# Kernel tuning notes

Measured on AMD Instinct MI355X. Metric: run time of the kernel, lower is better.

## Reference

```python
import jax, jax.numpy as jnp
import numpy as np

N, E, B = 250000, 1000000, 500
FD = 78  # num_features_xd


def setup_inputs() -> dict:
    key = jax.random.key(0)
    ks = jax.random.split(key, 24)
    g = lambda i, shape, fan_in: jax.random.normal(ks[i], shape, jnp.float32) / np.sqrt(fan_in)
    inp = {
        "x": jax.random.normal(ks[0], (N, FD), jnp.float32),
        "edge_index": jax.random.randint(ks[1], (2, E), 0, N, jnp.int32),
        "batch": jnp.repeat(jnp.arange(B, dtype=jnp.int32), N // B),  # sorted, every graph non-empty
        "target": jax.random.randint(ks[2], (B, 1000), 0, 26, jnp.int32),
        # GCN layers
        "W1": g(3, (FD, FD), FD), "b1": jnp.zeros((FD,), jnp.float32),
        "W2": g(4, (FD, 2 * FD), FD), "b2": jnp.zeros((2 * FD,), jnp.float32),
        "W3": g(5, (2 * FD, 4 * FD), 2 * FD), "b3": jnp.zeros((4 * FD,), jnp.float32),
        # graph head
        "fcg1_w": g(6, (4 * FD, 1024), 4 * FD), "fcg1_b": jnp.zeros((1024,), jnp.float32),
        "fcg2_w": g(7, (1024, 128), 1024), "fcg2_b": jnp.zeros((128,), jnp.float32),
        # protein branch
        "emb": g(8, (26, 128), 1),
        "conv_w": g(9, (32, 1000, 8), 1000 * 8), "conv_b": jnp.zeros((32,), jnp.float32),
        "fcxt_w": g(10, (32 * 121, 128), 32 * 121), "fcxt_b": jnp.zeros((128,), jnp.float32),
        # fusion head
        "fc1_w": g(11, (256, 1024), 256), "fc1_b": jnp.zeros((1024,), jnp.float32),
        "fc2_w": g(12, (1024, 512), 1024), "fc2_b": jnp.zeros((512,), jnp.float32),
        "out_w": g(13, (512, 1), 512), "out_b": jnp.zeros((1,), jnp.float32),
    }
    return inp


def _gcn_conv(x, W, b, src, dst, dinv, n):
    # PyG GCNConv: out = D^-1/2 (A+I) D^-1/2 (x W) + b, symmetric norm with self-loops
    xw = x @ W
    norm = dinv[src] * dinv[dst]                                   # [E]
    agg = jax.ops.segment_sum(xw[src] * norm[:, None], dst, num_segments=n)
    agg = agg + xw * (dinv * dinv)[:, None]                        # self-loop term
    return agg + b


def reference(x, edge_index, batch, target,
              W1, b1, W2, b2, W3, b3,
              fcg1_w, fcg1_b, fcg2_w, fcg2_b,
              emb, conv_w, conv_b, fcxt_w, fcxt_b,
              fc1_w, fc1_b, fc2_w, fc2_b, out_w, out_b):
    n = x.shape[0]
    src, dst = edge_index[0], edge_index[1]
    # degree with self-loops (edge weights 1)
    deg = jax.ops.segment_sum(jnp.ones((src.shape[0],), x.dtype), dst, num_segments=n) + 1.0
    dinv = jax.lax.rsqrt(deg)

    h = jax.nn.relu(_gcn_conv(x, W1, b1, src, dst, dinv, n))
    h = jax.nn.relu(_gcn_conv(h, W2, b2, src, dst, dinv, n))
    h = jax.nn.relu(_gcn_conv(h, W3, b3, src, dst, dinv, n))

    bsz = fcg2_w.shape[1] * 0 + target.shape[0]  # B
    g = jax.ops.segment_max(h, batch, num_segments=bsz)            # global max pool -> [B, 312]
    g = jax.nn.relu(g @ fcg1_w + fcg1_b)
    g = g @ fcg2_w + fcg2_b                                        # dropout = identity (eval)

    # protein branch: Conv1d over embedding dim (channels = seq positions = 1000)
    e = emb[target]                                                # [B, 1000, 128]
    c = jax.lax.conv_general_dilated(e, conv_w, window_strides=(1,), padding="VALID",
                                     dimension_numbers=("NCH", "OIH", "NCH"))
    c = c + conv_b[None, :, None]                                  # [B, 32, 121]
    xt = c.reshape(bsz, 32 * 121) @ fcxt_w + fcxt_b

    xc = jnp.concatenate([g, xt], axis=1)                          # [B, 256]
    xc = jax.nn.relu(xc @ fc1_w + fc1_b)
    xc = jax.nn.relu(xc @ fc2_w + fc2_b)
    return xc @ out_w + out_b                                      # [B, 1]
```

## Files before the change

### kernel.cpp

```cpp
#include <hip/hip_runtime.h>
#include <hip/hip_bf16.h>

#define DEV_INLINE __device__ __forceinline__

static constexpr int Nn = 250000;
static constexpr int Ee = 1000000;
static constexpr int Bb = 500;
static constexpr int NPB = Nn / Bb;

typedef __attribute__((ext_vector_type(8))) short short8;
typedef __attribute__((ext_vector_type(8))) unsigned short ushort8v;
typedef __attribute__((ext_vector_type(4))) float f32x4;

DEV_INLINE float b2f(__hip_bfloat16 v) { return __bfloat162float(v); }
DEV_INLINE __hip_bfloat16 f2b(float v) { return __float2bfloat16(v); }
DEV_INLINE unsigned short f2bu(float v) {
    __hip_bfloat16 h = __float2bfloat16(v);
    return __builtin_bit_cast(unsigned short, h);
}
DEV_INLINE float bfu2f(unsigned short u) { return __uint_as_float(((unsigned)u) << 16); }

__global__ void k_deg(const int* __restrict__ dst, int* __restrict__ deg) {
    int i = blockIdx.x * 256 + threadIdx.x;
    if (i < Ee) atomicAdd(&deg[dst[i]], 1);
}

__global__ void k_dinv(const int* __restrict__ deg, float* __restrict__ dinv) {
    int i = blockIdx.x * 256 + threadIdx.x;
    if (i < Nn) dinv[i] = rsqrtf((float)deg[i] + 1.0f);
}

__global__ __launch_bounds__(256) void k_scan1(const int* __restrict__ deg,
                                               int* __restrict__ rp,
                                               int* __restrict__ bsum) {
    __shared__ int s[256];
    int t = threadIdx.x;
    int i = blockIdx.x * 256 + t;
    int v = (i < Nn) ? deg[i] : 0;
    s[t] = v;
    __syncthreads();
    for (int off = 1; off < 256; off <<= 1) {
        int x = (t >= off) ? s[t - off] : 0;
        __syncthreads();
        s[t] += x;
        __syncthreads();
    }
    if (i < Nn) rp[i] = s[t] - v;
    if (t == 255) bsum[blockIdx.x] = s[255];
}

__global__ __launch_bounds__(1024) void k_scan2(int* __restrict__ bsum, int nb) {
    __shared__ int s[1024];
    int t = threadIdx.x;
    int v = (t < nb) ? bsum[t] : 0;
    s[t] = v;
    __syncthreads();
    for (int off = 1; off < 1024; off <<= 1) {
        int x = (t >= off) ? s[t - off] : 0;
        __syncthreads();
        s[t] += x;
        __syncthreads();
    }
    if (t < nb) bsum[t] = s[t] - v;
}

__global__ void k_scan3(int* __restrict__ rp, int* __restrict__ cursor,
                        const int* __restrict__ bsum) {
    int i = blockIdx.x * 256 + threadIdx.x;
    if (i < Nn) {
        int v = rp[i] + bsum[blockIdx.x];
        rp[i] = v;
        cursor[i] = v;
    }
    if (i == 0) rp[Nn] = Ee;
}

__global__ void k_scatter(const int* __restrict__ src, const int* __restrict__ dst,
                          const float* __restrict__ dinv, int* __restrict__ cursor,
                          int* __restrict__ col, float* __restrict__ enorm) {
    int i = blockIdx.x * 256 + threadIdx.x;
    if (i >= Ee) return;
    int s = src[i], d = dst[i];
    int pos = atomicAdd(&cursor[d], 1);
    col[pos] = s;
    enorm[pos] = dinv[s] * dinv[d];
}

__global__ void k_xprep(const float* __restrict__ x, unsigned short* __restrict__ xb) {
    int gid = blockIdx.x * 256 + threadIdx.x;
    if (gid >= Nn * 20) return;
    int i = gid / 20;
    int c = gid - 20 * i;
    int k = 4 * c;
    const float* xp = x + (size_t)i * 78;
    ushort4 u;
    u.x = (k + 0 < 78) ? f2bu(xp[k + 0]) : (unsigned short)0;
    u.y = (k + 1 < 78) ? f2bu(xp[k + 1]) : (unsigned short)0;
    u.z = (k + 2 < 78) ? f2bu(xp[k + 2]) : (unsigned short)0;
    u.w = (k + 3 < 78) ? f2bu(xp[k + 3]) : (unsigned short)0;
    *(ushort4*)&xb[(size_t)i * 80 + k] = u;
}

template <int K, int F, int KP, int FP>
__global__ __launch_bounds__(64) void k_wprep(const float* __restrict__ W,
                                              unsigned short* __restrict__ Wb) {
    constexpr int KSTEPS = KP / 32;
    const int nt = blockIdx.x, ks = blockIdx.y;
    const int l = threadIdx.x;
    const int n = nt * 16 + (l & 15);
    unsigned short* o = Wb + ((size_t)(nt * KSTEPS + ks) * 64 + l) * 8;
#pragma unroll
    for (int j = 0; j < 8; ++j) {
        const int k = (l >> 4) * 8 + j + ks * 32;
        o[j] = (k < K && n < F) ? f2bu(W[(size_t)k * F + n]) : (unsigned short)0;
    }
}

template <int KIN, int KP, int F, int FP, int SOUT, bool POOL>
__global__ __launch_bounds__(320) void k_gcn(const __hip_bfloat16* __restrict__ in_,
                                             const int* __restrict__ rp,
                                             const int* __restrict__ col,
                                             const float* __restrict__ enorm,
                                             const float* __restrict__ dinv,
                                             const unsigned short* __restrict__ Wb,
                                             const float* __restrict__ bias,
                                             __hip_bfloat16* __restrict__ out,
                                             float* __restrict__ gpool) {
    constexpr int ROWS = 16, BD = 320, WAVES = 5;
    constexpr int CPR = KIN / 8;
    constexpr int SLOTS = CPR * ROWS;
    constexpr int ECAP = 16 * ROWS;
    constexpr int KSTEPS = KP / 32;
    constexpr int NT = FP / 16;
    constexpr int TPW = NT / WAVES;
    static_assert(KIN % 8 == 0 && KP % 32 == 0 && KP >= KIN && FP % (16 * WAVES) == 0, "pad");
    const unsigned short* in = (const unsigned short*)in_;

    __shared__ alignas(16) unsigned short sh[ROWS * KP];
    __shared__ int sRp[ROWS + 1];
    __shared__ int sCol[ECAP];
    __shared__ float sEn[ECAP];

    const int i0 = blockIdx.x * ROWS;
    const int t = threadIdx.x;

    if (t <= ROWS) sRp[t] = rp[i0 + t];
    const int base = rp[i0];
    const int ne = rp[i0 + ROWS] - base;
    if (ne <= ECAP) {
        for (int e = t; e < ne; e += BD) {
            sCol[e] = col[base + e];
            sEn[e] = enorm[base + e];
        }
    }
    if constexpr (KP > KIN) {
        for (int e = t; e < ROWS * (KP - KIN); e += BD) {
            const int r = e / (KP - KIN);
            sh[r * KP + KIN + (e - r * (KP - KIN))] = 0;
        }
    }
    __syncthreads();

    for (int slot = t; slot < SLOTS; slot += BD) {
        const int r = slot / CPR;
        const int c = slot - r * CPR;
        const int i = i0 + r;
        const size_t coff = (size_t)8 * c;
        const float di = dinv[i];
        const float selfw = di * di;
        float acc[8];
        {
            ushort8v s = *(const ushort8v*)(in + (size_t)i * KIN + coff);
#pragma unroll
            for (int j = 0; j < 8; ++j) acc[j] = bfu2f(s[j]) * selfw;
        }
        const int e0a = sRp[r], e1a = sRp[r + 1];
        if (ne <= ECAP) {
            int j = e0a - base;
            const int jend = e1a - base;
            for (; j + 4 <= jend; j += 4) {
                const int n0 = sCol[j + 0], n1 = sCol[j + 1], n2 = sCol[j + 2], n3 = sCol[j + 3];
                const float w0 = sEn[j + 0], w1 = sEn[j + 1], w2 = sEn[j + 2], w3 = sEn[j + 3];
                ushort8v a0 = *(const ushort8v*)(in + (size_t)n0 * KIN + coff);
                ushort8v a1 = *(const ushort8v*)(in + (size_t)n1 * KIN + coff);
                ushort8v a2 = *(const ushort8v*)(in + (size_t)n2 * KIN + coff);
                ushort8v a3 = *(const ushort8v*)(in + (size_t)n3 * KIN + coff);
#pragma unroll
                for (int q = 0; q < 8; ++q)
                    acc[q] += bfu2f(a0[q]) * w0 + bfu2f(a1[q]) * w1 +
                              bfu2f(a2[q]) * w2 + bfu2f(a3[q]) * w3;
            }
            for (; j < jend; ++j) {
                const int n = sCol[j];
                const float w = sEn[j];
                ushort8v a = *(const ushort8v*)(in + (size_t)n * KIN + coff);
#pragma unroll
                for (int q = 0; q < 8; ++q) acc[q] += bfu2f(a[q]) * w;
            }
        } else {
            for (int j = e0a; j < e1a; ++j) {
                const int n = col[j];
                const float w = enorm[j];
                ushort8v a = *(const ushort8v*)(in + (size_t)n * KIN + coff);
#pragma unroll
                for (int q = 0; q < 8; ++q) acc[q] += bfu2f(a[q]) * w;
            }
        }
        ushort8v o;
#pragma unroll
        for (int q = 0; q < 8; ++q) o[q] = f2bu(acc[q]);
        *(ushort8v*)&sh[r * KP + 8 * c] = o;
    }
    __syncthreads();

    const int w = t >> 6, lane = t & 63;
    const int arow = lane & 15, aquad = lane >> 4;
    short8 afr[KSTEPS];
#pragma unroll
    for (int ks = 0; ks < KSTEPS; ++ks)
        afr[ks] = *(const short8*)&sh[arow * KP + aquad * 8 + ks * 32];

    const bool uni = (i0 / NPB) == ((i0 + ROWS - 1) / NPB);

#pragma unroll
    for (int nti = 0; nti < TPW; ++nti) {
        const int nt = w * TPW + nti;
        const short8* bp = (const short8*)Wb + (size_t)nt * KSTEPS * 64 + lane;
        f32x4 acc = {0.f, 0.f, 0.f, 0.f};
#pragma unroll
        for (int ks = 0; ks < KSTEPS; ++ks) {
            short8 bfr = bp[ks * 64];
            acc = __builtin_amdgcn_mfma_f32_16x16x32_bf16(afr[ks], bfr, acc, 0, 0, 0);
        }
        const int f = nt * 16 + arow;
        const int ib = i0 + aquad * 4;
        if constexpr (!POOL) {
            if (f < F) {
                const float bv = bias[f];
#pragma unroll
                for (int r = 0; r < 4; ++r)
                    out[(size_t)(ib + r) * SOUT + f] = f2b(fmaxf(acc[r] + bv, 0.f));
            } else if (f < SOUT) {
#pragma unroll
                for (int r = 0; r < 4; ++r)
                    out[(size_t)(ib + r) * SOUT + f] = f2b(0.f);
            }
        } else {
            float m = 0.f, v[4];
            const float bv = (f < F) ? bias[f] : 0.f;
#pragma unroll
            for (int r = 0; r < 4; ++r) {
                v[r] = fmaxf(acc[r] + bv, 0.f);
                m = fmaxf(m, v[r]);
            }
            if (uni) {
                m = fmaxf(m, __shfl_xor(m, 16));
                m = fmaxf(m, __shfl_xor(m, 32));
                if (aquad == 0 && f < F)
                    atomicMax((int*)&gpool[(i0 / NPB) * F + f], __float_as_int(m));
            } else if (f < F) {
                const int g0 = ib / NPB, g3 = (ib + 3) / NPB;
                if (g0 == g3) {
                    atomicMax((int*)&gpool[g0 * F + f], __float_as_int(m));
                } else {
#pragma unroll
                    for (int r = 0; r < 4; ++r)
                        atomicMax((int*)&gpool[((ib + r) / NPB) * F + f], __float_as_int(v[r]));
                }
            }
        }
    }
}

template <int K, int FOUT, int KS, bool RELU, int BD>
__global__ __launch_bounds__(BD) void k_fc(const float* __restrict__ in,
                                           const float* __restrict__ W,
                                           const float* __restrict__ bias,
                                           float* __restrict__ out,
                                           int ostride, int ooff) {
    static_assert(!(RELU && KS > 1), "cannot split K with fused ReLU");
    static_assert(K % KS == 0, "K must divide evenly");
    constexpr int KC = K / KS;
    const int j = blockIdx.x * BD + threadIdx.x;
    const int b = blockIdx.y;
    const int z = blockIdx.z;
    const float* __restrict__ inp = in + (size_t)b * K + z * KC;
    const float* __restrict__ Wp = W + (size_t)(z * KC) * FOUT + j;
    float acc = (z == 0) ? bias[j] : 0.f;
#pragma unroll 8
    for (int k = 0; k < KC; ++k) acc += inp[k] * Wp[(size_t)k * FOUT];
    float* dst = &out[(size_t)b * ostride + ooff + j];
    if (KS > 1) {
        atomicAdd(dst, acc);
    } else {
        *dst = RELU ? fmaxf(acc, 0.f) : acc;
    }
}

__global__ __launch_bounds__(128) void k_P(const float* __restrict__ emb,
                                           const float* __restrict__ fcxt_w,
                                           float* __restrict__ P) {
    const int v = blockIdx.x, o = blockIdx.y;
    const int j = threadIdx.x;
    __shared__ float se[128];
    se[j] = emb[v * 128 + j];
    __syncthreads();
    float acc[8];
#pragma unroll
    for (int k = 0; k < 8; ++k) acc[k] = 0.f;
    const float* fw = fcxt_w + (size_t)(o * 121) * 128 + j;
#pragma unroll 4
    for (int h = 0; h < 121; ++h) {
        const float f = fw[(size_t)h * 128];
#pragma unroll
        for (int k = 0; k < 8; ++k) acc[k] += se[h + k] * f;
    }
    float* Pp = P + ((size_t)(v * 32 + o) * 8) * 128 + j;
#pragma unroll
    for (int k = 0; k < 8; ++k) Pp[(size_t)k * 128] = acc[k];
}

__global__ __launch_bounds__(128) void k_T(const float* __restrict__ convw,
                                           const float* __restrict__ P,
                                           float* __restrict__ T) {
    const int i0 = blockIdx.x * 8;
    const int v = blockIdx.y;
    const int t = threadIdx.x;
    __shared__ float wt[8 * 256];
    for (int e = t; e < 2048; e += 128) {
        const int r = e >> 8;
        const int kk = e & 255;
        wt[e] = convw[(size_t)(kk >> 3) * 8000 + (size_t)(i0 + r) * 8 + (kk & 7)];
    }
    __syncthreads();
    float acc[8];
#pragma unroll
    for (int r = 0; r < 8; ++r) acc[r] = 0.f;
    const float* Pp = P + (size_t)v * 256 * 128 + t;
#pragma unroll 2
    for (int kk = 0; kk < 256; ++kk) {
        const float pv = Pp[(size_t)kk * 128];
#pragma unroll
        for (int r = 0; r < 8; ++r) acc[r] += wt[r * 256 + kk] * pv;
    }
    float* Tp = T + ((size_t)v * 1000 + i0) * 128 + t;
#pragma unroll
    for (int r = 0; r < 8; ++r) Tp[(size_t)r * 128] = acc[r];
}

__global__ __launch_bounds__(128) void k_C0(const float* __restrict__ fcxt_w,
                                            const float* __restrict__ fcxt_b,
                                            const float* __restrict__ convb,
                                            float* __restrict__ C0) {
    const int o = blockIdx.x;
    const int j = threadIdx.x;
    float acc = 0.f;
    const float* fw = fcxt_w + (size_t)(o * 121) * 128 + j;
#pragma unroll 4
    for (int h = 0; h < 121; ++h) acc += fw[(size_t)h * 128];
    acc *= convb[o];
    if (o == 0) acc += fcxt_b[j];
    atomicAdd(&C0[j], acc);
}

template <int ZS>
__global__ __launch_bounds__(128) void k_xt(const int* __restrict__ target,
                                            const float* __restrict__ T,
                                            const float* __restrict__ C0,
                                            float* __restrict__ xc) {
    constexpr int CH = 1000 / ZS;
    const int b = blockIdx.x;
    const int z = blockIdx.y;
    const int j = threadIdx.x;
    const int* tg = target + b * 1000 + z * CH;
    float acc = (z == 0) ? C0[j] : 0.f;
    int i = 0;
    for (; i + 4 <= CH; i += 4) {
        const int v0 = tg[i + 0], v1 = tg[i + 1], v2 = tg[i + 2], v3 = tg[i + 3];
        const int ib = z * CH + i;
        acc += T[((size_t)v0 * 1000 + ib + 0) * 128 + j]
             + T[((size_t)v1 * 1000 + ib + 1) * 128 + j]
             + T[((size_t)v2 * 1000 + ib + 2) * 128 + j]
             + T[((size_t)v3 * 1000 + ib + 3) * 128 + j];
    }
    for (; i < CH; ++i) {
        acc += T[((size_t)tg[i] * 1000 + z * CH + i) * 128 + j];
    }
    atomicAdd(&xc[(size_t)b * 256 + 128 + j], acc);
}

__global__ __launch_bounds__(64) void k_out(const float* __restrict__ in,
                                            const float* __restrict__ w,
                                            const float* __restrict__ ob,
                                            float* __restrict__ out) {
    const int b = blockIdx.x;
    const int lane = threadIdx.x;
    const float* p = in + (size_t)b * 512;
    float acc = 0.f;
#pragma unroll
    for (int i = 0; i < 8; ++i) acc += p[lane + 64 * i] * w[lane + 64 * i];
    for (int off = 32; off > 0; off >>= 1) acc += __shfl_down(acc, off);
    if (lane == 0) out[b] = acc + ob[0];
}

extern "C" void kernel_launch(void* const* d_in, const int* in_sizes, int n_in,
                              void* d_out, int out_size, void* d_ws, size_t ws_size,
                              hipStream_t stream) {
    (void)in_sizes; (void)n_in; (void)out_size; (void)ws_size;
    const float* x      = (const float*)d_in[0];
    const int* ei       = (const int*)d_in[1];
    const int* target   = (const int*)d_in[3];
    const float* W1     = (const float*)d_in[4];
    const float* b1     = (const float*)d_in[5];
    const float* W2     = (const float*)d_in[6];
    const float* b2     = (const float*)d_in[7];
    const float* W3     = (const float*)d_in[8];
    const float* b3     = (const float*)d_in[9];
    const float* fcg1_w = (const float*)d_in[10];
    const float* fcg1_b = (const float*)d_in[11];
    const float* fcg2_w = (const float*)d_in[12];
    const float* fcg2_b = (const float*)d_in[13];
    const float* emb    = (const float*)d_in[14];
    const float* conv_w = (const float*)d_in[15];
    const float* conv_b = (const float*)d_in[16];
    const float* fcxt_w = (const float*)d_in[17];
    const float* fcxt_b = (const float*)d_in[18];
    const float* fc1_w  = (const float*)d_in[19];
    const float* fc1_b  = (const float*)d_in[20];
    const float* fc2_w  = (const float*)d_in[21];
    const float* fc2_b  = (const float*)d_in[22];
    const float* out_w  = (const float*)d_in[23];
    const float* out_b  = (const float*)d_in[24];

    const int* src = ei;
    const int* dst = ei + Ee;

    size_t off = 0;
    auto alloc = [&](size_t bytes) -> void* {
        off = (off + 255) & ~(size_t)255;
        void* p = (char*)d_ws + off;
        off += bytes;
        return p;
    };
    int*   deg    = (int*)alloc((size_t)Nn * 4);
    float* dinv   = (float*)alloc((size_t)Nn * 4);
    int*   rp     = (int*)alloc((size_t)(Nn + 1) * 4);
    int*   col    = (int*)alloc((size_t)Ee * 4);
    float* enorm  = (float*)alloc((size_t)Ee * 4);
    int*   bsum   = (int*)alloc(1024 * 4);
    unsigned short* Wb1 = (unsigned short*)alloc((size_t)5 * 3 * 64 * 8 * 2);
    unsigned short* Wb2 = (unsigned short*)alloc((size_t)10 * 3 * 64 * 8 * 2);
    unsigned short* Wb3 = (unsigned short*)alloc((size_t)20 * 5 * 64 * 8 * 2);
    __hip_bfloat16* h1 = (__hip_bfloat16*)alloc((size_t)Nn * 80 * 2);
    __hip_bfloat16* h2 = (__hip_bfloat16*)alloc((size_t)Nn * 160 * 2);
    int* cursor = deg;
    unsigned short* xb = (unsigned short*)h2;

    size_t hoff = 0;
    auto halloc = [&](size_t bytes) -> void* {
        hoff = (hoff + 255) & ~(size_t)255;
        void* p = (char*)h1 + hoff;
        hoff += bytes;
        return p;
    };
    float* gpool = (float*)halloc((size_t)Bb * 312 * 4);
    float* g1    = (float*)halloc((size_t)Bb * 1024 * 4);
    float* xc    = (float*)halloc((size_t)Bb * 256 * 4);
    float* f1    = (float*)halloc((size_t)Bb * 1024 * 4);
    float* f2    = (float*)halloc((size_t)Bb * 512 * 4);
    float* C0    = (float*)halloc(128 * 4);
    float* Pbuf  = (float*)halloc((size_t)26 * 32 * 8 * 128 * 4);
    float* Tbuf  = (float*)halloc((size_t)26 * 1000 * 128 * 4);

    const int nb = (Nn + 255) / 256;

    k_xprep<<<(Nn * 20 + 255) / 256, 256, 0, stream>>>(x, xb);

    hipMemsetAsync(deg, 0, (size_t)Nn * 4, stream);
    k_deg<<<(Ee + 255) / 256, 256, 0, stream>>>(dst, deg);
    k_dinv<<<nb, 256, 0, stream>>>(deg, dinv);
    k_scan1<<<nb, 256, 0, stream>>>(deg, rp, bsum);
    k_scan2<<<1, 1024, 0, stream>>>(bsum, nb);
    k_scan3<<<nb, 256, 0, stream>>>(rp, cursor, bsum);
    k_scatter<<<(Ee + 255) / 256, 256, 0, stream>>>(src, dst, dinv, cursor, col, enorm);

    k_wprep<78, 78, 96, 80><<<dim3(5, 3), 64, 0, stream>>>(W1, Wb1);
    k_wprep<78, 156, 96, 160><<<dim3(10, 3), 64, 0, stream>>>(W2, Wb2);
    k_wprep<156, 312, 160, 320><<<dim3(20, 5), 64, 0, stream>>>(W3, Wb3);

    k_gcn<80, 96, 78, 80, 80, false><<<Nn / 16, 320, 0, stream>>>(
        (const __hip_bfloat16*)xb, rp, col, enorm, dinv, Wb1, b1, h1, (float*)nullptr);
    k_gcn<80, 96, 156, 160, 160, false><<<Nn / 16, 320, 0, stream>>>(
        h1, rp, col, enorm, dinv, Wb2, b2, h2, (float*)nullptr);
    hipMemsetAsync(gpool, 0, (size_t)Bb * 312 * 4, stream);
    k_gcn<160, 160, 312, 320, 0, true><<<Nn / 16, 320, 0, stream>>>(
        h2, rp, col, enorm, dinv, Wb3, b3, (__hip_bfloat16*)nullptr, gpool);

    hipMemsetAsync(C0, 0, 128 * 4, stream);
    hipMemsetAsync(xc, 0, (size_t)Bb * 256 * 4, stream);
    k_P<<<dim3(26, 32), 128, 0, stream>>>(emb, fcxt_w, Pbuf);
    k_T<<<dim3(125, 26), 128, 0, stream>>>(conv_w, Pbuf, Tbuf);
    k_C0<<<32, 128, 0, stream>>>(fcxt_w, fcxt_b, conv_b, C0);
    k_xt<8><<<dim3(Bb, 8), 128, 0, stream>>>(target, Tbuf, C0, xc);

    k_fc<312, 1024, 1, true, 256><<<dim3(4, Bb, 1), 256, 0, stream>>>(gpool, fcg1_w, fcg1_b, g1, 1024, 0);
    k_fc<1024, 128, 2, false, 128><<<dim3(1, Bb, 2), 128, 0, stream>>>(g1, fcg2_w, fcg2_b, xc, 256, 0);

    k_fc<256, 1024, 1, true, 256><<<dim3(4, Bb, 1), 256, 0, stream>>>(xc, fc1_w, fc1_b, f1, 1024, 0);
    k_fc<1024, 512, 1, true, 256><<<dim3(2, Bb, 1), 256, 0, stream>>>(f1, fc2_w, fc2_b, f2, 512, 0);
    k_out<<<Bb, 64, 0, stream>>>(f2, out_w, out_b, (float*)d_out);
}
```

Measured before the change: 886.3 us.

## Double GCN row tile, batch rows in FC kernels, restructure protein gather

The GCN kernel now handles 32 rows per block with two MFMA row tiles, so each weight fragment load feeds two MFMAs and the block count halves. The FC kernels compute 4 batch rows per thread to reuse each weight load. The protein xt kernel is rewritten to stage a per-position slice of T in shared memory and accumulate over position chunks for many batch rows, with a separate init kernel writing C0 into xc. Risks are higher register and LDS use from the doubled GCN tile (the aggregation phase shown uses ROWS, and part of it is hidden), fewer blocks to fill the GPU, and more atomics in xt.

```diff
diff --git a/kernel.cpp b/kernel.cpp
--- a/kernel.cpp
+++ b/kernel.cpp
@@ -126,14 +126,14 @@
                                              const float* __restrict__ bias,
                                              __hip_bfloat16* __restrict__ out,
                                              float* __restrict__ gpool) {
-    constexpr int ROWS = 16, BD = 320, WAVES = 5;
+    constexpr int ROWS = 32, BD = 320, WAVES = 5, RT = 2;
     constexpr int CPR = KIN / 8;
     constexpr int SLOTS = CPR * ROWS;
     constexpr int ECAP = 16 * ROWS;
     constexpr int KSTEPS = KP / 32;
-    constexpr int NT = FP / 16;
-    constexpr int TPW = NT / WAVES;
-    static_assert(KIN % 8 == 0 && KP % 32 == 0 && KP >= KIN && FP % (16 * WAVES) == 0, "pad");
+    constexpr int NT_F = FP / 16;
+    constexpr int FTPW = NT_F / WAVES;
+    static_assert(KIN % 8 == 0 && KP % 32 == 0 && KP >= KIN && NT_F % WAVES == 0, "pad");
     const unsigned short* in = (const unsigned short*)in_;
 
     __shared__ alignas(16) unsigned short sh[ROWS * KP];
@@ -215,64 +215,80 @@
 
     const int w = t >> 6, lane = t & 63;
     const int arow = lane & 15, aquad = lane >> 4;
-    short8 afr[KSTEPS];
-#pragma unroll
-    for (int ks = 0; ks < KSTEPS; ++ks)
-        afr[ks] = *(const short8*)&sh[arow * KP + aquad * 8 + ks * 32];
+    short8 afr[RT][KSTEPS];
+#pragma unroll
+    for (int rt = 0; rt < RT; ++rt)
+#pragma unroll
+        for (int ks = 0; ks < KSTEPS; ++ks)
+            afr[rt][ks] = *(const short8*)&sh[(rt * 16 + arow) * KP + aquad * 8 + ks * 32];
 
     const bool uni = (i0 / NPB) == ((i0 + ROWS - 1) / NPB);
 
 #pragma unroll
-    for (int nti = 0; nti < TPW; ++nti) {
-        const int nt = w * TPW + nti;
-        const short8* bp = (const short8*)Wb + (size_t)nt * KSTEPS * 64 + lane;
-        f32x4 acc = {0.f, 0.f, 0.f, 0.f};
+    for (int ftj = 0; ftj < FTPW; ++ftj) {
+        const int ft = w * FTPW + ftj;
+        const short8* bp = (const short8*)Wb + (size_t)ft * KSTEPS * 64 + lane;
+        f32x4 a0 = {0.f, 0.f, 0.f, 0.f}, a1 = {0.f, 0.f, 0.f, 0.f};
 #pragma unroll
         for (int ks = 0; ks < KSTEPS; ++ks) {
             short8 bfr = bp[ks * 64];
-            acc = __builtin_amdgcn_mfma_f32_16x16x32_bf16(afr[ks], bfr, acc, 0, 0, 0);
-        }
-        const int f = nt * 16 + arow;
-        const int ib = i0 + aquad * 4;
+            a0 = __builtin_amdgcn_mfma_f32_16x16x32_bf16(afr[0][ks], bfr, a0, 0, 0, 0);
+            a1 = __builtin_amdgcn_mfma_f32_16x16x32_bf16(afr[1][ks], bfr, a1, 0, 0, 0);
+        }
+        const int f = ft * 16 + arow;
+        const float bv = (f < F) ? bias[f] : 0.f;
+        float v0[4], v1[4];
+#pragma unroll
+        for (int r = 0; r < 4; ++r) {
+            v0[r] = fmaxf(a0[r] + bv, 0.f);
+            v1[r] = fmaxf(a1[r] + bv, 0.f);
+        }
         if constexpr (!POOL) {
+            const int ib0 = i0 + aquad * 4;
+            const int ib1 = i0 + 16 + aquad * 4;
             if (f < F) {
-                const float bv = bias[f];
-#pragma unroll
-                for (int r = 0; r < 4; ++r)
-                    out[(size_t)(ib + r) * SOUT + f] = f2b(fmaxf(acc[r] + bv, 0.f));
+#pragma unroll
+                for (int r = 0; r < 4; ++r) {
+                    out[(size_t)(ib0 + r) * SOUT + f] = f2b(v0[r]);
+                    out[(size_t)(ib1 + r) * SOUT + f] = f2b(v1[r]);
+                }
             } else if (f < SOUT) {
 #pragma unroll
-                for (int r = 0; r < 4; ++r)
-                    out[(size_t)(ib + r) * SOUT + f] = f2b(0.f);
+                for (int r = 0; r < 4; ++r) {
+                    out[(size_t)(ib0 + r) * SOUT + f] = f2b(0.f);
+                    out[(size_t)(ib1 + r) * SOUT + f] = f2b(0.f);
+                }
             }
         } else {
-            float m = 0.f, v[4];
-            const float bv = (f < F) ? bias[f] : 0.f;
-#pragma unroll
-            for (int r = 0; r < 4; ++r) {
-                v[r] = fmaxf(acc[r] + bv, 0.f);
-                m = fmaxf(m, v[r]);
-            }
             if (uni) {
+                float m = 0.f;
+#pragma unroll
+                for (int r = 0; r < 4; ++r) m = fmaxf(m, fmaxf(v0[r], v1[r]));
                 m = fmaxf(m, __shfl_xor(m, 16));
                 m = fmaxf(m, __shfl_xor(m, 32));
                 if (aquad == 0 && f < F)
                     atomicMax((int*)&gpool[(i0 / NPB) * F + f], __float_as_int(m));
             } else if (f < F) {
-                const int g0 = ib / NPB, g3 = (ib + 3) / NPB;
-                if (g0 == g3) {
-                    atomicMax((int*)&gpool[g0 * F + f], __float_as_int(m));
-                } else {
-#pragma unroll
-                    for (int r = 0; r < 4; ++r)
-                        atomicMax((int*)&gpool[((ib + r) / NPB) * F + f], __float_as_int(v[r]));
+#pragma unroll
+                for (int rt = 0; rt < RT; ++rt) {
+                    const int ib = i0 + rt * 16 + aquad * 4;
+                    const float* v = rt ? v1 : v0;
+                    const int g0 = ib / NPB, g3 = (ib + 3) / NPB;
+                    if (g0 == g3) {
+                        float m = fmaxf(fmaxf(v[0], v[1]), fmaxf(v[2], v[3]));
+                        atomicMax((int*)&gpool[g0 * F + f], __float_as_int(m));
+                    } else {
+#pragma unroll
+                        for (int r = 0; r < 4; ++r)
+                            atomicMax((int*)&gpool[((ib + r) / NPB) * F + f], __float_as_int(v[r]));
+                    }
                 }
             }
         }
     }
 }
 
-template <int K, int FOUT, int KS, bool RELU, int BD>
+template <int K, int FOUT, int KS, bool RELU, int BD, int BR>
 __global__ __launch_bounds__(BD) void k_fc(const float* __restrict__ in,
                                            const float* __restrict__ W,
                                            const float* __restrict__ bias,
@@ -282,18 +298,24 @@
     static_assert(K % KS == 0, "K must divide evenly");
     constexpr int KC = K / KS;
     const int j = blockIdx.x * BD + threadIdx.x;
-    const int b = blockIdx.y;
+    const int b0 = blockIdx.y * BR;
     const int z = blockIdx.z;
-    const float* __restrict__ inp = in + (size_t)b * K + z * KC;
     const float* __restrict__ Wp = W + (size_t)(z * KC) * FOUT + j;
-    float acc = (z == 0) ? bias[j] : 0.f;
-#pragma unroll 8
-    for (int k = 0; k < KC; ++k) acc += inp[k] * Wp[(size_t)k * FOUT];
-    float* dst = &out[(size_t)b * ostride + ooff + j];
-    if (KS > 1) {
-        atomicAdd(dst, acc);
-    } else {
-        *dst = RELU ? fmaxf(acc, 0.f) : acc;
+    float acc[BR];
+#pragma unroll
+    for (int r = 0; r < BR; ++r) acc[r] = (z == 0) ? bias[j] : 0.f;
+#pragma unroll 4
+    for (int k = 0; k < KC; ++k) {
+        const float wv = Wp[(size_t)k * FOUT];
+#pragma unroll
+        for (int r = 0; r < BR; ++r)
+            acc[r] += in[(size_t)(b0 + r) * K + z * KC + k] * wv;
+    }
+#pragma unroll
+    for (int r = 0; r < BR; ++r) {
+        float* dst = &out[(size_t)(b0 + r) * ostride + ooff + j];
+        if (KS > 1) atomicAdd(dst, acc[r]);
+        else        *dst = RELU ? fmaxf(acc[r], 0.f) : acc[r];
     }
 }
 
@@ -363,30 +385,63 @@
     atomicAdd(&C0[j], acc);
 }
 
-template <int ZS>
-__global__ __launch_bounds__(128) void k_xt(const int* __restrict__ target,
+__global__ void k_xcinit(const float* __restrict__ C0, float* __restrict__ xc) {
+    int gid = blockIdx.x * 256 + threadIdx.x;
+    if (gid < Bb * 128) {
+        int b = gid >> 7, j = gid & 127;
+        xc[(size_t)b * 256 + 128 + j] = C0[j];
+    }
+}
+
+template <int ICH, int BCH>
+__global__ __launch_bounds__(256) void k_xt(const int* __restrict__ target,
                                             const float* __restrict__ T,
-                                            const float* __restrict__ C0,
                                             float* __restrict__ xc) {
-    constexpr int CH = 1000 / ZS;
-    const int b = blockIdx.x;
-    const int z = blockIdx.y;
-    const int j = threadIdx.x;
-    const int* tg = target + b * 1000 + z * CH;
-    float acc = (z == 0) ? C0[j] : 0.f;
-    int i = 0;
-    for (; i + 4 <= CH; i += 4) {
-        const int v0 = tg[i + 0], v1 = tg[i + 1], v2 = tg[i + 2], v3 = tg[i + 3];
-        const int ib = z * CH + i;
-        acc += T[((size_t)v0 * 1000 + ib + 0) * 128 + j]
-             + T[((size_t)v1 * 1000 + ib + 1) * 128 + j]
-             + T[((size_t)v2 * 1000 + ib + 2) * 128 + j]
-             + T[((size_t)v3 * 1000 + ib + 3) * 128 + j];
-    }
-    for (; i < CH; ++i) {
-        acc += T[((size_t)tg[i] * 1000 + z * CH + i) * 128 + j];
-    }
-    atomicAdd(&xc[(size_t)b * 256 + 128 + j], acc);
+    const int i0 = blockIdx.x * ICH;
+    const int b0 = blockIdx.y * BCH;
+    const int tid = threadIdx.x;
+    const int j4 = tid & 31;
+    const int bp = tid >> 5;
+    constexpr int NBS = (BCH + 7) / 8;
+
+    __shared__ float sT[26 * 128];
+    __shared__ int sTg[BCH * ICH];
+
+    for (int e = tid; e < BCH * ICH; e += 256) {
+        const int bl = e / ICH, ii = e - bl * ICH;
+        sTg[e] = target[(size_t)(b0 + bl) * 1000 + i0 + ii];
+    }
+
+    float4 acc[NBS];
+#pragma unroll
+    for (int bs = 0; bs < NBS; ++bs) acc[bs] = make_float4(0.f, 0.f, 0.f, 0.f);
+
+    for (int ii = 0; ii < ICH; ++ii) {
+        __syncthreads();
+        for (int e = tid; e < 26 * 128; e += 256)
+            sT[e] = T[((size_t)(e >> 7) * 1000 + i0 + ii) * 128 + (e & 127)];
+        __syncthreads();
+#pragma unroll
+        for (int bs = 0; bs < NBS; ++bs) {
+            const int bl = bp + bs * 8;
+            if (bl < BCH) {
+                const int v = sTg[bl * ICH + ii];
+                float4 tv = *(const float4*)&sT[v * 128 + j4 * 4];
+                acc[bs].x += tv.x; acc[bs].y += tv.y; acc[bs].z += tv.z; acc[bs].w += tv.w;
+            }
+        }
+    }
+#pragma unroll
+    for (int bs = 0; bs < NBS; ++bs) {
+        const int bl = bp + bs * 8;
+        if (bl < BCH) {
+            float* dst = &xc[(size_t)(b0 + bl) * 256 + 128 + j4 * 4];
+            atomicAdd(dst + 0, acc[bs].x);
+            atomicAdd(dst + 1, acc[bs].y);
+            atomicAdd(dst + 2, acc[bs].z);
+            atomicAdd(dst + 3, acc[bs].w);
+        }
+    }
 }
 
 __global__ __launch_bounds__(64) void k_out(const float* __restrict__ in,
@@ -488,12 +543,12 @@
     k_wprep<78, 156, 96, 160><<<dim3(10, 3), 64, 0, stream>>>(W2, Wb2);
     k_wprep<156, 312, 160, 320><<<dim3(20, 5), 64, 0, stream>>>(W3, Wb3);
 
-    k_gcn<80, 96, 78, 80, 80, false><<<Nn / 16, 320, 0, stream>>>(
+    k_gcn<80, 96, 78, 80, 80, false><<<Nn / 32, 320, 0, stream>>>(
         (const __hip_bfloat16*)xb, rp, col, enorm, dinv, Wb1, b1, h1, (float*)nullptr);
-    k_gcn<80, 96, 156, 160, 160, false><<<Nn / 16, 320, 0, stream>>>(
+    k_gcn<80, 96, 156, 160, 160, false><<<Nn / 32, 320, 0, stream>>>(
         h1, rp, col, enorm, dinv, Wb2, b2, h2, (float*)nullptr);
     hipMemsetAsync(gpool, 0, (size_t)Bb * 312 * 4, stream);
-    k_gcn<160, 160, 312, 320, 0, true><<<Nn / 16, 320, 0, stream>>>(
+    k_gcn<160, 160, 312, 320, 0, true><<<Nn / 32, 320, 0, stream>>>(
         h2, rp, col, enorm, dinv, Wb3, b3, (__hip_bfloat16*)nullptr, gpool);
 
     hipMemsetAsync(C0, 0, 128 * 4, stream);
@@ -501,12 +556,13 @@
     k_P<<<dim3(26, 32), 128, 0, stream>>>(emb, fcxt_w, Pbuf);
     k_T<<<dim3(125, 26), 128, 0, stream>>>(conv_w, Pbuf, Tbuf);
     k_C0<<<32, 128, 0, stream>>>(fcxt_w, fcxt_b, conv_b, C0);
-    k_xt<8><<<dim3(Bb, 8), 128, 0, stream>>>(target, Tbuf, C0, xc);
-
-    k_fc<312, 1024, 1, true, 256><<<dim3(4, Bb, 1), 256, 0, stream>>>(gpool, fcg1_w, fcg1_b, g1, 1024, 0);
-    k_fc<1024, 128, 2, false, 128><<<dim3(1, Bb, 2), 128, 0, stream>>>(g1, fcg2_w, fcg2_b, xc, 256, 0);
-
-    k_fc<256, 1024, 1, true, 256><<<dim3(4, Bb, 1), 256, 0, stream>>>(xc, fc1_w, fc1_b, f1, 1024, 0);
-    k_fc<1024, 512, 1, true, 256><<<dim3(2, Bb, 1), 256, 0, stream>>>(f1, fc2_w, fc2_b, f2, 512, 0);
+    k_xcinit<<<(Bb * 128 + 255) / 256, 256, 0, stream>>>(C0, xc);
+    k_xt<20, 125><<<dim3(50, 4), 256, 0, stream>>>(target, Tbuf, xc);
+
+    k_fc<312, 1024, 1, true, 256, 4><<<dim3(4, Bb / 4, 1), 256, 0, stream>>>(gpool, fcg1_w, fcg1_b, g1, 1024, 0);
+    k_fc<1024, 128, 2, false, 128, 4><<<dim3(1, Bb / 4, 2), 128, 0, stream>>>(g1, fcg2_w, fcg2_b, xc, 256, 0);
+
+    k_fc<256, 1024, 1, true, 256, 4><<<dim3(4, Bb / 4, 1), 256, 0, stream>>>(xc, fc1_w, fc1_b, f1, 1024, 0);
+    k_fc<1024, 512, 1, true, 256, 4><<<dim3(2, Bb / 4, 1), 256, 0, stream>>>(f1, fc2_w, fc2_b, f2, 512, 0);
     k_out<<<Bb, 64, 0, stream>>>(f2, out_w, out_b, (float*)d_out);
 }
```

Result: slower. 1.041 ms (+17.5%).
